# Kernel tuning notes

Measured on AMD Instinct MI355X. Metric: run time of the kernel, lower is better.

Reference implementation:

```python
import jax, jax.numpy as jnp
import numpy as np

B, D_IN, D_OUT = 16384, 1024, 1024


def setup_inputs() -> dict:
    key = jax.random.key(0)
    ks = jax.random.split(key, 14)
    s_x = 1.0 / np.sqrt(D_IN)
    s_h = 1.0 / np.sqrt(D_OUT)
    inp = {
        "inputs": jax.random.normal(ks[0], (B, D_IN), dtype=jnp.float32),
        "hist": jax.random.normal(ks[1], (B, D_OUT), dtype=jnp.float32),
        "carousel": 1,
    }
    names = ["f", "i", "o", "c"]
    for g, n in enumerate(names):
        inp[f"W{n}x"] = jax.random.normal(ks[2 + 3 * g], (D_IN, D_OUT), dtype=jnp.float32) * s_x
        inp[f"W{n}h"] = jax.random.normal(ks[3 + 3 * g], (D_OUT, D_OUT), dtype=jnp.float32) * s_h
        inp[f"b{n}"] = jnp.zeros((D_OUT,), dtype=jnp.float32)
    return inp


def reference(inputs, hist, carousel, Wfx, Wfh, bf, Wix, Wih, bi, Wox, Woh, bo, Wcx, Wch, bc):
    # Each GateMirrored: act(x @ Wx + h @ Wh + b)
    def gate(Wx, Wh, b, act):
        return act(inputs @ Wx + hist @ Wh + b)

    f = gate(Wfx, Wfh, bf, jax.nn.sigmoid)
    i = gate(Wix, Wih, bi, jax.nn.sigmoid)
    o = gate(Wox, Woh, bo, jax.nn.sigmoid)
    g = gate(Wcx, Wch, bc, jnp.tanh)

    c = f * jnp.float32(carousel) + i * g
    h = o * c
    return (h, c)
```

## Files before the change

kernel.cpp:

```cpp
#include <hip/hip_runtime.h>
#include <stdint.h>
#include <stddef.h>

#define B_ROWS 16384
#define DIN 1024
#define DOUT 1024
#define KDIM 2048

#define BM 128
#define BNP 128
#define BK 64

typedef __bf16 bf16x8 __attribute__((ext_vector_type(8)));
typedef float floatx4 __attribute__((ext_vector_type(4)));

__device__ __forceinline__ unsigned short f2bf(float f) {
  unsigned int u = __float_as_uint(f);
  u += 0x7fffu + ((u >> 16) & 1u);
  return (unsigned short)(u >> 16);
}

__device__ __forceinline__ void async16(const void* g, void* l) {
  __builtin_amdgcn_global_load_lds(
      (__attribute__((address_space(1))) void*)(g),
      (__attribute__((address_space(3))) void*)(l), 16, 0, 0);
}

__device__ __forceinline__ float sigmoid_f(float x) {
  return 1.0f / (1.0f + __expf(-x));
}
__device__ __forceinline__ float tanh_f(float x) {
  return 2.0f / (1.0f + __expf(-2.0f * x)) - 1.0f;
}

__global__ void cast_x_kernel(const float* __restrict__ inp,
                              const float* __restrict__ hist,
                              unsigned short* __restrict__ xb) {
  int idx = blockIdx.x * blockDim.x + threadIdx.x;
  const int per = B_ROWS * DIN / 4;
  const float* src;
  int colOff;
  int i = idx;
  if (i < per) { src = inp; colOff = 0; }
  else         { src = hist; colOff = DIN; i -= per; }
  int e = i * 4;
  int row = e >> 10;
  int col = e & 1023;
  const float4 v = *(const float4*)(src + (size_t)row * 1024 + col);
  ushort4 o;
  o.x = f2bf(v.x); o.y = f2bf(v.y); o.z = f2bf(v.z); o.w = f2bf(v.w);
  *(ushort4*)(xb + (size_t)row * KDIM + colOff + col) = o;
}

__global__ void transpose_cast_kernel(
    const float* __restrict__ s0, const float* __restrict__ s1,
    const float* __restrict__ s2, const float* __restrict__ s3,
    const float* __restrict__ s4, const float* __restrict__ s5,
    const float* __restrict__ s6, const float* __restrict__ s7,
    unsigned short* __restrict__ wt) {
  __shared__ float tile[32][33];
  const int z = blockIdx.z;
  const float* src;
  switch (z) {
    case 0: src = s0; break; case 1: src = s1; break;
    case 2: src = s2; break; case 3: src = s3; break;
    case 4: src = s4; break; case 5: src = s5; break;
    case 6: src = s6; break; default: src = s7; break;
  }
  const int g = z >> 1, part = z & 1;
  const int tx = threadIdx.x, ty = threadIdx.y;
  const int n0 = blockIdx.x * 32, k0 = blockIdx.y * 32;
#pragma unroll
  for (int j = 0; j < 32; j += 8)
    tile[ty + j][tx] = src[(size_t)(k0 + ty + j) * DOUT + n0 + tx];
  __syncthreads();
#pragma unroll
  for (int j = 0; j < 32; j += 8) {
    const int n = n0 + ty + j;
    const int np = (n >> 5) * 128 + g * 32 + (n & 31);
    wt[(size_t)np * KDIM + part * DIN + k0 + tx] = f2bf(tile[tx][ty + j]);
  }
}

__global__ __launch_bounds__(256, 3) void lstm_fused_kernel(
    const unsigned short* __restrict__ Xb,
    const unsigned short* __restrict__ Wt2,
    const float* __restrict__ b_f, const float* __restrict__ b_i,
    const float* __restrict__ b_o, const float* __restrict__ b_c,
    const int* __restrict__ carousel,
    float* __restrict__ out) {
  __shared__ unsigned short As[BM * BK];
  __shared__ unsigned short Bs[BNP * BK];

  const int tid  = threadIdx.x;
  const int lane = tid & 63;
  const int wave = tid >> 6;
  const int wm   = wave * 32;
  const int m16  = lane & 15;
  const int quad = lane >> 4;
  const int r7   = m16 & 7;
  const int bm   = blockIdx.y * BM;
  const int cg   = blockIdx.x;

  const unsigned short* Wp = Wt2 + (size_t)cg * BNP * KDIM;

  floatx4 acc[2][8];
#pragma unroll
  for (int mi = 0; mi < 2; ++mi)
#pragma unroll
    for (int ni = 0; ni < 8; ++ni)
      acc[mi][ni] = (floatx4){0.f, 0.f, 0.f, 0.f};

  int srow[4], scol[4];
#pragma unroll
  for (int j = 0; j < 4; ++j) {
    const int c = j * 256 + tid;
    srow[j] = c >> 3;
    scol[j] = (c & 7) ^ (srow[j] & 7);
  }

  for (int kt = 0; kt < KDIM; kt += BK) {
#pragma unroll
    for (int j = 0; j < 4; ++j) {
      const int c = j * 256 + tid;
      async16(Xb + (size_t)(bm + srow[j]) * KDIM + kt + scol[j] * 8, As + c * 8);
    }
#pragma unroll
    for (int j = 0; j < 4; ++j) {
      const int c = j * 256 + tid;
      async16(Wp + (size_t)srow[j] * KDIM + kt + scol[j] * 8, Bs + c * 8);
    }
    __syncthreads();
#pragma unroll
    for (int kk = 0; kk < 2; ++kk) {
      const int t = (kk * 4 + quad) ^ r7;
      bf16x8 av[2], bv[8];
#pragma unroll
      for (int mi = 0; mi < 2; ++mi)
        av[mi] = *(const bf16x8*)(As + (wm + mi * 16 + m16) * BK + t * 8);
#pragma unroll
      for (int ni = 0; ni < 8; ++ni)
        bv[ni] = *(const bf16x8*)(Bs + (ni * 16 + m16) * BK + t * 8);
#pragma unroll
      for (int mi = 0; mi < 2; ++mi)
#pragma unroll
        for (int ni = 0; ni < 8; ++ni)
          acc[mi][ni] = __builtin_amdgcn_mfma_f32_16x16x32_bf16(
              av[mi], bv[ni], acc[mi][ni], 0, 0, 0);
    }
    __syncthreads();
  }

  const float cf = (float)carousel[0];
  float bfv[2], biv[2], bov[2], bcv[2];
#pragma unroll
  for (int cs = 0; cs < 2; ++cs) {
    const int col = cg * 32 + cs * 16 + m16;
    bfv[cs] = b_f[col]; biv[cs] = b_i[col];
    bov[cs] = b_o[col]; bcv[cs] = b_c[col];
  }

#pragma unroll
  for (int mi = 0; mi < 2; ++mi) {
#pragma unroll
    for (int cs = 0; cs < 2; ++cs) {
      const int col = cg * 32 + cs * 16 + m16;
#pragma unroll
      for (int r = 0; r < 4; ++r) {
        const int row = bm + wm + mi * 16 + quad * 4 + r;
        const float f = sigmoid_f(acc[mi][0 + cs][r] + bfv[cs]);
        const float i = sigmoid_f(acc[mi][2 + cs][r] + biv[cs]);
        const float o = sigmoid_f(acc[mi][4 + cs][r] + bov[cs]);
        const float g = tanh_f   (acc[mi][6 + cs][r] + bcv[cs]);
        const float c = f * cf + i * g;
        const float h = o * c;
        out[(size_t)row * DOUT + col] = h;
        out[(size_t)(B_ROWS * DOUT) + (size_t)row * DOUT + col] = c;
      }
    }
  }
}

extern "C" void kernel_launch(void* const* d_in, const int* in_sizes, int n_in,
                              void* d_out, int out_size, void* d_ws, size_t ws_size,
                              hipStream_t stream) {
  const float* inputs = (const float*)d_in[0];
  const float* hist   = (const float*)d_in[1];
  const int* carousel = (const int*)d_in[2];
  const float* Wfx = (const float*)d_in[3];
  const float* Wfh = (const float*)d_in[4];
  const float* bfv = (const float*)d_in[5];
  const float* Wix = (const float*)d_in[6];
  const float* Wih = (const float*)d_in[7];
  const float* biv = (const float*)d_in[8];
  const float* Wox = (const float*)d_in[9];
  const float* Woh = (const float*)d_in[10];
  const float* bov = (const float*)d_in[11];
  const float* Wcx = (const float*)d_in[12];
  const float* Wch = (const float*)d_in[13];
  const float* bcv = (const float*)d_in[14];

  unsigned short* Xb  = (unsigned short*)d_ws;
  unsigned short* Wt2 = Xb + (size_t)B_ROWS * KDIM;

  {
    const int total = 2 * B_ROWS * DIN / 4;
    cast_x_kernel<<<total / 256, 256, 0, stream>>>(inputs, hist, Xb);
  }
  {
    dim3 grid(DOUT / 32, DIN / 32, 8);
    dim3 block(32, 8);
    transpose_cast_kernel<<<grid, block, 0, stream>>>(
        Wfx, Wfh, Wix, Wih, Wox, Woh, Wcx, Wch, Wt2);
  }
  {
    dim3 grid(DOUT / 32, B_ROWS / BM);
    lstm_fused_kernel<<<grid, 256, 0, stream>>>(
        Xb, Wt2, bfv, biv, bov, bcv, carousel, (float*)d_out);
  }
}
```

Measured before the change: 520.3 us.

## Rewrite LSTM GEMM with 256x256 tiles, double-buffered async pipeline, and merged prep kernel

Merges the activation cast and weight transpose-cast into a single prep launch, with the gate interleave regrouped to 16 columns. The fused GEMM now uses 256x256 tiles with 512 threads and split-K halves in double-buffered LDS. Global-to-LDS copies are software-pipelined with explicit vmcnt waits, barriers and setprio around MFMA bursts. The aim is more reuse per tile, loads overlapped with MFMA work, and one fewer launch. The cost is heavier register and LDS use, which allows fewer blocks per CU.

Measured after the change: 520.6 us. No clear change (+0.0%).

```diff
diff --git a/kernel.cpp b/kernel.cpp
--- a/kernel.cpp
+++ b/kernel.cpp
@@ -7,8 +7,8 @@
 #define DOUT 1024
 #define KDIM 2048
 
-#define BM 128
-#define BNP 128
+#define BM 256
+#define BNP 256
 #define BK 64
 
 typedef __bf16 bf16x8 __attribute__((ext_vector_type(8)));
@@ -33,33 +33,34 @@
   return 2.0f / (1.0f + __expf(-2.0f * x)) - 1.0f;
 }
 
-__global__ void cast_x_kernel(const float* __restrict__ inp,
-                              const float* __restrict__ hist,
-                              unsigned short* __restrict__ xb) {
-  int idx = blockIdx.x * blockDim.x + threadIdx.x;
-  const int per = B_ROWS * DIN / 4;
-  const float* src;
-  int colOff;
-  int i = idx;
-  if (i < per) { src = inp; colOff = 0; }
-  else         { src = hist; colOff = DIN; i -= per; }
-  int e = i * 4;
-  int row = e >> 10;
-  int col = e & 1023;
-  const float4 v = *(const float4*)(src + (size_t)row * 1024 + col);
-  ushort4 o;
-  o.x = f2bf(v.x); o.y = f2bf(v.y); o.z = f2bf(v.z); o.w = f2bf(v.w);
-  *(ushort4*)(xb + (size_t)row * KDIM + colOff + col) = o;
-}
-
-__global__ void transpose_cast_kernel(
+__global__ void prep_kernel(
+    const float* __restrict__ inp, const float* __restrict__ hist,
     const float* __restrict__ s0, const float* __restrict__ s1,
     const float* __restrict__ s2, const float* __restrict__ s3,
     const float* __restrict__ s4, const float* __restrict__ s5,
     const float* __restrict__ s6, const float* __restrict__ s7,
-    unsigned short* __restrict__ wt) {
+    unsigned short* __restrict__ xb, unsigned short* __restrict__ wt) {
   __shared__ float tile[32][33];
-  const int z = blockIdx.z;
+  const int tid = threadIdx.x;
+  if (blockIdx.x < 32768) {
+    int idx = blockIdx.x * 256 + tid;
+    const int per = B_ROWS * DIN / 4;
+    const float* src;
+    int colOff;
+    int i = idx;
+    if (i < per) { src = inp; colOff = 0; }
+    else         { src = hist; colOff = DIN; i -= per; }
+    int e = i * 4;
+    int row = e >> 10;
+    int col = e & 1023;
+    const float4 v = *(const float4*)(src + (size_t)row * 1024 + col);
+    ushort4 o;
+    o.x = f2bf(v.x); o.y = f2bf(v.y); o.z = f2bf(v.z); o.w = f2bf(v.w);
+    *(ushort4*)(xb + (size_t)row * KDIM + colOff + col) = o;
+    return;
+  }
+  const int bb = blockIdx.x - 32768;
+  const int bx = bb & 31, by = (bb >> 5) & 31, z = bb >> 10;
   const float* src;
   switch (z) {
     case 0: src = s0; break; case 1: src = s1; break;
@@ -68,8 +69,8 @@
     case 6: src = s6; break; default: src = s7; break;
   }
   const int g = z >> 1, part = z & 1;
-  const int tx = threadIdx.x, ty = threadIdx.y;
-  const int n0 = blockIdx.x * 32, k0 = blockIdx.y * 32;
+  const int tx = tid & 31, ty = tid >> 5;
+  const int n0 = bx * 32, k0 = by * 32;
 #pragma unroll
   for (int j = 0; j < 32; j += 8)
     tile[ty + j][tx] = src[(size_t)(k0 + ty + j) * DOUT + n0 + tx];
@@ -77,106 +78,165 @@
 #pragma unroll
   for (int j = 0; j < 32; j += 8) {
     const int n = n0 + ty + j;
-    const int np = (n >> 5) * 128 + g * 32 + (n & 31);
+    const int np = ((n >> 4) << 6) + g * 16 + (n & 15);
     wt[(size_t)np * KDIM + part * DIN + k0 + tx] = f2bf(tile[tx][ty + j]);
   }
 }
 
-__global__ __launch_bounds__(256, 3) void lstm_fused_kernel(
+#define FENCE() __builtin_amdgcn_sched_barrier(0)
+#define BAR() do { FENCE(); __builtin_amdgcn_s_barrier(); FENCE(); } while (0)
+#define WAITV(N) asm volatile("s_waitcnt vmcnt(" #N ")" ::: "memory")
+#define REGOFF(BUF, KH) (((BUF) * 2 + (KH)) << 13)
+
+#define STAGE_A(BUF, KH, KT) do {                                          \
+    unsigned short* d_ = As + REGOFF(BUF, KH) + tid * 8;                   \
+    async16(agA + (KT) + (KH) * 32, d_);                                   \
+    async16(agA + 128 * KDIM + (KT) + (KH) * 32, d_ + 4096);               \
+  } while (0)
+#define STAGE_B(BUF, KH, KT) do {                                          \
+    unsigned short* d_ = Bs + REGOFF(BUF, KH) + tid * 8;                   \
+    async16(agB + (KT) + (KH) * 32, d_);                                   \
+    async16(agB + 128 * KDIM + (KT) + (KH) * 32, d_ + 4096);               \
+  } while (0)
+#define LDA4(BUF, KK, MH) do {                                             \
+    const unsigned short* b_ = As + REGOFF(BUF, KK) + (MH) * 2048 + aoff;  \
+    _Pragma("unroll")                                                      \
+    for (int mi = 0; mi < 4; ++mi)                                         \
+      av[mi] = *(const bf16x8*)(b_ + mi * 512);                            \
+  } while (0)
+#define LDB4(BUF, KK) do {                                                 \
+    const unsigned short* b_ = Bs + REGOFF(BUF, KK) + boff;                \
+    _Pragma("unroll")                                                      \
+    for (int ni = 0; ni < 4; ++ni)                                         \
+      bv[ni] = *(const bf16x8*)(b_ + ni * 512);                            \
+  } while (0)
+#define MFMA16(MH) do {                                                    \
+    __builtin_amdgcn_s_setprio(1);                                         \
+    _Pragma("unroll")                                                      \
+    for (int mi = 0; mi < 4; ++mi)                                         \
+      _Pragma("unroll")                                                    \
+      for (int ni = 0; ni < 4; ++ni)                                       \
+        acc[(MH) * 4 + mi][ni] = __builtin_amdgcn_mfma_f32_16x16x32_bf16(  \
+            av[mi], bv[ni], acc[(MH) * 4 + mi][ni], 0, 0, 0);              \
+    __builtin_amdgcn_s_setprio(0);                                         \
+  } while (0)
+
+__global__ __launch_bounds__(512, 2) void lstm_fused_kernel(
     const unsigned short* __restrict__ Xb,
     const unsigned short* __restrict__ Wt2,
     const float* __restrict__ b_f, const float* __restrict__ b_i,
     const float* __restrict__ b_o, const float* __restrict__ b_c,
     const int* __restrict__ carousel,
     float* __restrict__ out) {
-  __shared__ unsigned short As[BM * BK];
-  __shared__ unsigned short Bs[BNP * BK];
+  __shared__ unsigned short As[4 * 256 * 32];
+  __shared__ unsigned short Bs[4 * 256 * 32];
 
   const int tid  = threadIdx.x;
   const int lane = tid & 63;
   const int wave = tid >> 6;
-  const int wm   = wave * 32;
+  const int wr   = wave >> 2;
+  const int wc   = wave & 3;
   const int m16  = lane & 15;
   const int quad = lane >> 4;
-  const int r7   = m16 & 7;
+  const int ua   = quad ^ ((m16 >> 1) & 3);
   const int bm   = blockIdx.y * BM;
   const int cg   = blockIdx.x;
 
   const unsigned short* Wp = Wt2 + (size_t)cg * BNP * KDIM;
 
-  floatx4 acc[2][8];
-#pragma unroll
-  for (int mi = 0; mi < 2; ++mi)
-#pragma unroll
-    for (int ni = 0; ni < 8; ++ni)
+  const int col = cg * 64 + wc * 16 + m16;
+  const float bfv = b_f[col], biv = b_i[col], bov = b_o[col], bcv = b_c[col];
+  const float cf  = (float)carousel[0];
+  FENCE();
+
+  const int srow   = tid >> 2;
+  const int schunk = (tid & 3) ^ ((srow >> 1) & 3);
+  const unsigned short* agA = Xb + (size_t)(bm + srow) * KDIM + schunk * 8;
+  const unsigned short* agB = Wp + (size_t)srow * KDIM + schunk * 8;
+
+  const int aoff = (wr * 128 + m16) * 32 + ua * 8;
+  const int boff = (wc * 64 + m16) * 32 + ua * 8;
+
+  floatx4 acc[8][4];
+#pragma unroll
+  for (int mi = 0; mi < 8; ++mi)
+#pragma unroll
+    for (int ni = 0; ni < 4; ++ni)
       acc[mi][ni] = (floatx4){0.f, 0.f, 0.f, 0.f};
 
-  int srow[4], scol[4];
-#pragma unroll
-  for (int j = 0; j < 4; ++j) {
-    const int c = j * 256 + tid;
-    srow[j] = c >> 3;
-    scol[j] = (c & 7) ^ (srow[j] & 7);
-  }
-
-  for (int kt = 0; kt < KDIM; kt += BK) {
-#pragma unroll
-    for (int j = 0; j < 4; ++j) {
-      const int c = j * 256 + tid;
-      async16(Xb + (size_t)(bm + srow[j]) * KDIM + kt + scol[j] * 8, As + c * 8);
-    }
-#pragma unroll
-    for (int j = 0; j < 4; ++j) {
-      const int c = j * 256 + tid;
-      async16(Wp + (size_t)srow[j] * KDIM + kt + scol[j] * 8, Bs + c * 8);
-    }
-    __syncthreads();
-#pragma unroll
-    for (int kk = 0; kk < 2; ++kk) {
-      const int t = (kk * 4 + quad) ^ r7;
-      bf16x8 av[2], bv[8];
-#pragma unroll
-      for (int mi = 0; mi < 2; ++mi)
-        av[mi] = *(const bf16x8*)(As + (wm + mi * 16 + m16) * BK + t * 8);
-#pragma unroll
-      for (int ni = 0; ni < 8; ++ni)
-        bv[ni] = *(const bf16x8*)(Bs + (ni * 16 + m16) * BK + t * 8);
-#pragma unroll
-      for (int mi = 0; mi < 2; ++mi)
-#pragma unroll
-        for (int ni = 0; ni < 8; ++ni)
-          acc[mi][ni] = __builtin_amdgcn_mfma_f32_16x16x32_bf16(
-              av[mi], bv[ni], acc[mi][ni], 0, 0, 0);
-    }
-    __syncthreads();
-  }
-
-  const float cf = (float)carousel[0];
-  float bfv[2], biv[2], bov[2], bcv[2];
-#pragma unroll
-  for (int cs = 0; cs < 2; ++cs) {
-    const int col = cg * 32 + cs * 16 + m16;
-    bfv[cs] = b_f[col]; biv[cs] = b_i[col];
-    bov[cs] = b_o[col]; bcv[cs] = b_c[col];
-  }
-
-#pragma unroll
-  for (int mi = 0; mi < 2; ++mi) {
-#pragma unroll
-    for (int cs = 0; cs < 2; ++cs) {
-      const int col = cg * 32 + cs * 16 + m16;
-#pragma unroll
-      for (int r = 0; r < 4; ++r) {
-        const int row = bm + wm + mi * 16 + quad * 4 + r;
-        const float f = sigmoid_f(acc[mi][0 + cs][r] + bfv[cs]);
-        const float i = sigmoid_f(acc[mi][2 + cs][r] + biv[cs]);
-        const float o = sigmoid_f(acc[mi][4 + cs][r] + bov[cs]);
-        const float g = tanh_f   (acc[mi][6 + cs][r] + bcv[cs]);
-        const float c = f * cf + i * g;
-        const float h = o * c;
-        out[(size_t)row * DOUT + col] = h;
-        out[(size_t)(B_ROWS * DOUT) + (size_t)row * DOUT + col] = c;
-      }
+  bf16x8 av[4], bv[4];
+
+  STAGE_B(0, 0, 0);
+  STAGE_A(0, 0, 0);
+  STAGE_B(0, 1, 0);
+  STAGE_A(0, 1, 0);
+  STAGE_B(1, 0, 64);
+  STAGE_A(1, 0, 64);
+  STAGE_B(1, 1, 64);
+  WAITV(10);
+  BAR();
+
+#pragma unroll 1
+  for (int p = 0; p < 15; ++p) {
+    const int kt = p * 128;
+    LDA4(0, 0, 0); LDB4(0, 0);
+    STAGE_A(1, 1, kt + 64);
+    BAR(); MFMA16(0); BAR();
+    LDA4(0, 0, 1);
+    STAGE_B(0, 0, kt + 128);
+    WAITV(10); BAR(); MFMA16(1); BAR();
+    LDA4(0, 1, 0); LDB4(0, 1);
+    STAGE_A(0, 0, kt + 128);
+    BAR(); MFMA16(0); BAR();
+    LDA4(0, 1, 1);
+    STAGE_B(0, 1, kt + 128);
+    WAITV(10); BAR(); MFMA16(1); BAR();
+    LDA4(1, 0, 0); LDB4(1, 0);
+    STAGE_A(0, 1, kt + 128);
+    BAR(); MFMA16(0); BAR();
+    LDA4(1, 0, 1);
+    STAGE_B(1, 0, kt + 192);
+    WAITV(10); BAR(); MFMA16(1); BAR();
+    LDA4(1, 1, 0); LDB4(1, 1);
+    STAGE_A(1, 0, kt + 192);
+    BAR(); MFMA16(0); BAR();
+    LDA4(1, 1, 1);
+    STAGE_B(1, 1, kt + 192);
+    WAITV(10); BAR(); MFMA16(1); BAR();
+  }
+
+  LDA4(0, 0, 0); LDB4(0, 0);
+  STAGE_A(1, 1, 1984);
+  BAR(); MFMA16(0); BAR();
+  LDA4(0, 0, 1);
+  WAITV(8); BAR(); MFMA16(1); BAR();
+  LDA4(0, 1, 0); LDB4(0, 1);
+  BAR(); MFMA16(0); BAR();
+  LDA4(0, 1, 1);
+  WAITV(4); BAR(); MFMA16(1); BAR();
+  LDA4(1, 0, 0); LDB4(1, 0);
+  BAR(); MFMA16(0); BAR();
+  LDA4(1, 0, 1);
+  WAITV(0); BAR(); MFMA16(1); BAR();
+  LDA4(1, 1, 0); LDB4(1, 1);
+  MFMA16(0);
+  LDA4(1, 1, 1);
+  MFMA16(1);
+
+  const int rbase = bm + wr * 128 + quad * 4;
+#pragma unroll
+  for (int mi = 0; mi < 8; ++mi) {
+#pragma unroll
+    for (int r = 0; r < 4; ++r) {
+      const int row = rbase + mi * 16 + r;
+      const float f = sigmoid_f(acc[mi][0][r] + bfv);
+      const float i = sigmoid_f(acc[mi][1][r] + biv);
+      const float o = sigmoid_f(acc[mi][2][r] + bov);
+      const float g = tanh_f   (acc[mi][3][r] + bcv);
+      const float c = f * cf + i * g;
+      const float h = o * c;
+      out[(size_t)row * DOUT + col] = h;
+      out[(size_t)(B_ROWS * DOUT) + (size_t)row * DOUT + col] = c;
     }
   }
 }
@@ -203,19 +263,10 @@
   unsigned short* Xb  = (unsigned short*)d_ws;
   unsigned short* Wt2 = Xb + (size_t)B_ROWS * KDIM;
 
-  {
-    const int total = 2 * B_ROWS * DIN / 4;
-    cast_x_kernel<<<total / 256, 256, 0, stream>>>(inputs, hist, Xb);
-  }
-  {
-    dim3 grid(DOUT / 32, DIN / 32, 8);
-    dim3 block(32, 8);
-    transpose_cast_kernel<<<grid, block, 0, stream>>>(
-        Wfx, Wfh, Wix, Wih, Wox, Woh, Wcx, Wch, Wt2);
-  }
-  {
-    dim3 grid(DOUT / 32, B_ROWS / BM);
-    lstm_fused_kernel<<<grid, 256, 0, stream>>>(
-        Xb, Wt2, bfv, biv, bov, bcv, carousel, (float*)d_out);
-  }
-}
+  prep_kernel<<<40960, 256, 0, stream>>>(
+      inputs, hist, Wfx, Wfh, Wix, Wih, Wox, Woh, Wcx, Wch, Xb, Wt2);
+
+  dim3 grid(16, B_ROWS / BM);
+  lstm_fused_kernel<<<grid, 512, 0, stream>>>(
+      Xb, Wt2, bfv, biv, bov, bcv, carousel, (float*)d_out);
+}
```
